# Kernel optimization log

Hardware: AMD Instinct MI355X
Metric: run time of the kernel (lower is better)

## Reference

```python
import jax, jax.numpy as jnp
import numpy as np

B, S, D, H, L, FF, V, T = 4, 160, 512, 8, 2, 2048, 50000, 256
Wd = D // H


def layer_norm(x, g, b, eps=1e-12):
    u = x.mean(-1, keepdims=True)
    s = ((x - u) ** 2).mean(-1, keepdims=True)
    return g * (x - u) / jnp.sqrt(s + eps) + b


def setup_inputs() -> dict:
    key = jax.random.key(0)
    ks = jax.random.split(key, 16)
    sc = 0.02
    inp = {
        'x': jax.random.randint(ks[0], (B, S), 0, V),
        'stamp': jax.random.randint(ks[1], (B, S - 1, 3), 0, 8),
        'mask': jnp.ones((B, S), dtype=jnp.int32),
        'time_matrix': jax.random.randint(ks[2], (B, S, S), 0, T + 1),
        'tok_emb': jax.random.normal(ks[3], (V, D)) * sc,
        'month_emb': jax.random.normal(ks[4], (13, D)) * sc,
        'day_emb': jax.random.normal(ks[5], (32, D)) * sc,
        'tiK_emb': jax.random.normal(ks[6], (T + 1, D)) * sc,
        'tiV_emb': jax.random.normal(ks[7], (T + 1, D)) * sc,
        'g0': jnp.ones((D,)), 'b0': jnp.zeros((D,)),
        'Wq': jax.random.normal(ks[8], (L, D, D)) * sc, 'bq': jnp.zeros((L, D)),
        'Wk': jax.random.normal(ks[9], (L, D, D)) * sc, 'bk': jnp.zeros((L, D)),
        'Wv': jax.random.normal(ks[10], (L, D, D)) * sc, 'bv': jnp.zeros((L, D)),
        'Wo': jax.random.normal(ks[11], (L, D, D)) * sc, 'bo': jnp.zeros((L, D)),
        'g1': jnp.ones((L, D)), 'b1': jnp.zeros((L, D)),
        'W1': jax.random.normal(ks[12], (L, D, FF)) * sc, 'c1': jnp.zeros((L, FF)),
        'W2': jax.random.normal(ks[13], (L, FF, D)) * sc, 'c2': jnp.zeros((L, D)),
        'g2': jnp.ones((L, D)), 'b2': jnp.zeros((L, D)),
    }
    return inp


def reference(x, stamp, mask, time_matrix, tok_emb, month_emb, day_emb,
              tiK_emb, tiV_emb, g0, b0, Wq, bq, Wk, bk, Wv, bv, Wo, bo,
              g1, b1, W1, c1, W2, c2, g2, b2):
    # Embeddings: month + day temporal embed, one zero timestep prepended
    t_e = month_emb[stamp[..., 0]] + day_emb[stamp[..., 1]]          # [B,S-1,D]
    t_e = jnp.concatenate([jnp.zeros((B, 1, D), t_e.dtype), t_e], axis=1)
    h = layer_norm(tok_emb[x] + t_e, g0, b0)                         # [B,S,D]
    tK = tiK_emb[time_matrix].reshape(B, S, S, H, Wd)                # [B,S,S,H,W]
    tV = tiV_emb[time_matrix].reshape(B, S, S, H, Wd)
    maskf = mask.astype(h.dtype)
    # faithful to original: +10000*(1-mask), added AFTER scaling
    bias = 10000.0 * (1.0 - maskf)[:, None, None, :]
    inv_sqrt = 1.0 / jnp.sqrt(jnp.asarray(Wd, h.dtype))
    for l in range(L):
        q = (h @ Wq[l] + bq[l]).reshape(B, S, H, Wd).transpose(0, 2, 1, 3)  # [B,H,S,W]
        k = (h @ Wk[l] + bk[l]).reshape(B, S, H, Wd).transpose(0, 2, 1, 3)
        v = (h @ Wv[l] + bv[l]).reshape(B, S, H, Wd).transpose(0, 2, 1, 3)
        scores = (jnp.einsum('bhiw,bhjw->bhij', q, k)
                  + jnp.einsum('bijhw,bhiw->bhij', tK, q)) * inv_sqrt + bias
        attn = jax.nn.softmax(scores, axis=-1)                        # [B,H,S,S]
        # standard value mix + diagonal of attn-weighted t_V (relative-time values)
        hh = (jnp.einsum('bhij,bhjw->bihw', attn, v)
              + jnp.einsum('bhik,bikhw->bihw', attn, tV)).reshape(B, S, D)
        h = layer_norm(h + hh @ Wo[l] + bo[l], g1[l], b1[l])
        ff = jax.nn.gelu(h @ W1[l] + c1[l], approximate=False) @ W2[l] + c2[l]
        h = layer_norm(h + ff, g2[l], b2[l])
    return h
```

## Files before the change

kernel.cpp:

```cpp
#include <hip/hip_runtime.h>
#include <hip/hip_bf16.h>
#include <math.h>

#define SS 160
#define DD 512
#define HH 8
#define MTOK 640
#define FFD 2048
#define NTT 257

typedef __attribute__((ext_vector_type(8))) short bfrag8;
typedef __attribute__((ext_vector_type(4))) float facc4;
typedef unsigned short u16;

#define SWZ(row, cb) ((cb) ^ (((row)&7) << 4))

__device__ __forceinline__ void gload16(const void* g, void* l) {
  __builtin_amdgcn_global_load_lds(
      (const __attribute__((address_space(1))) void*)g,
      (__attribute__((address_space(3))) void*)l, 16, 0, 0);
}

__device__ __forceinline__ u16 f2b(float f) {
  __hip_bfloat16 hb = __float2bfloat16(f);
  return *reinterpret_cast<u16*>(&hb);
}

__device__ void wconv_body(const float* __restrict__ src,
                           __hip_bfloat16* __restrict__ dst,
                           int K, int N, int dls, int rowoff,
                           int l, int bx, int by, float (*tile)[65])
{
  src += (size_t)l * K * N;
  dst += (size_t)l * dls + (size_t)rowoff * K;
  int k0 = by * 64, n0 = bx * 64;
  int t = threadIdx.x;
  int r = t >> 2, c0 = (t & 3) * 16;
  #pragma unroll
  for (int j = 0; j < 16; j += 4) {
    float4 v4 = *(const float4*)&src[(size_t)(k0 + r) * N + n0 + c0 + j];
    tile[r][c0 + j + 0] = v4.x; tile[r][c0 + j + 1] = v4.y;
    tile[r][c0 + j + 2] = v4.z; tile[r][c0 + j + 3] = v4.w;
  }
  __syncthreads();
  union { u16 u[8]; uint4 v; } pk;
  #pragma unroll
  for (int half = 0; half < 2; ++half) {
    #pragma unroll
    for (int j = 0; j < 8; ++j)
      pk.u[j] = f2b(tile[c0 + half * 8 + j][r]);
    *(uint4*)&dst[(size_t)(n0 + r) * K + k0 + c0 + half * 8] = pk.v;
  }
}

__global__ __launch_bounds__(256) void prep_all(
    const float* __restrict__ Wq, const float* __restrict__ Wk,
    const float* __restrict__ Wv, const float* __restrict__ Wo,
    const float* __restrict__ W1, const float* __restrict__ W2,
    const float* __restrict__ tiK,
    __hip_bfloat16* __restrict__ wqkv, __hip_bfloat16* __restrict__ wo_t,
    __hip_bfloat16* __restrict__ w1_t, __hip_bfloat16* __restrict__ w2_t,
    __hip_bfloat16* __restrict__ tikb,
    const int* __restrict__ x, const int* __restrict__ stamp,
    const float* __restrict__ tok, const float* __restrict__ month,
    const float* __restrict__ day, const float* __restrict__ g0,
    const float* __restrict__ b0, float* __restrict__ h,
    __hip_bfloat16* __restrict__ hb)
{
  __shared__ float tile[64][65];
  __shared__ float ssh[4], qsh[4];
  int idx = blockIdx.x;
  int tid = threadIdx.x;

  if (idx < 1536) {
    if (idx < 384) {
      int grp = idx / 128, r = idx % 128;
      int l = r / 64, t = r % 64;
      const float* src = grp == 0 ? Wq : (grp == 1 ? Wk : Wv);
      wconv_body(src, wqkv, 512, 512, 1536 * 512, 512 * grp, l, t % 8, t / 8, tile);
    } else if (idx < 512) {
      int r = idx - 384; int l = r / 64, t = r % 64;
      wconv_body(Wo, wo_t, 512, 512, 512 * 512, 0, l, t % 8, t / 8, tile);
    } else if (idx < 1024) {
      int r = idx - 512; int l = r / 256, t = r % 256;
      wconv_body(W1, w1_t, 512, 2048, 2048 * 512, 0, l, t % 32, t / 32, tile);
    } else {
      int r = idx - 1024; int l = r / 256, t = r % 256;
      wconv_body(W2, w2_t, 2048, 512, 512 * 2048, 0, l, t % 8, t / 8, tile);
    }
  } else if (idx < 1665) {
    int i = (idx - 1536) * 256 + tid;
    if (i < NTT * DD / 4) {
      float4 v = *(const float4*)(tiK + (size_t)i * 4);
      union { u16 u[4]; uint2 w; } pk;
      pk.u[0] = f2b(v.x); pk.u[1] = f2b(v.y);
      pk.u[2] = f2b(v.z); pk.u[3] = f2b(v.w);
      *(uint2*)(tikb + (size_t)i * 4) = pk.w;
    }
  } else {
    int m = idx - 1665;
    int b = m / SS, s = m % SS, t = tid;
    int tokid = x[m];
    float v0 = tok[tokid * DD + t];
    float v1 = tok[tokid * DD + t + 256];
    if (s > 0) {
      int sidx = (b * (SS - 1) + (s - 1)) * 3;
      int mo = stamp[sidx + 0], dy = stamp[sidx + 1];
      v0 += month[mo * DD + t]       + day[dy * DD + t];
      v1 += month[mo * DD + t + 256] + day[dy * DD + t + 256];
    }
    float sum = v0 + v1, sq = v0 * v0 + v1 * v1;
    #pragma unroll
    for (int off = 1; off < 64; off <<= 1) {
      sum += __shfl_xor(sum, off);
      sq  += __shfl_xor(sq , off);
    }
    if ((t & 63) == 0) { ssh[t >> 6] = sum; qsh[t >> 6] = sq; }
    __syncthreads();
    float fsum = ssh[0] + ssh[1] + ssh[2] + ssh[3];
    float fsq  = qsh[0] + qsh[1] + qsh[2] + qsh[3];
    float u = fsum * (1.0f / 512.0f);
    float var = fsq * (1.0f / 512.0f) - u * u;
    float r = rsqrtf(var + 1e-12f);
    float y0 = g0[t]       * ((v0 - u) * r) + b0[t];
    float y1 = g0[t + 256] * ((v1 - u) * r) + b0[t + 256];
    h[m * DD + t]        = y0;  h[m * DD + t + 256]  = y1;
    hb[m * DD + t]       = __float2bfloat16(y0);
    hb[m * DD + t + 256] = __float2bfloat16(y1);
  }
}

__global__ __launch_bounds__(256) void ln_kernel(
    const float* __restrict__ in, const float* __restrict__ g,
    const float* __restrict__ b, float* __restrict__ out,
    __hip_bfloat16* __restrict__ outb)
{
  int m = blockIdx.x; int t = threadIdx.x;
  float v0 = in[m*DD + t];
  float v1 = in[m*DD + t + 256];
  float sum = v0+v1, sq = v0*v0+v1*v1;
  #pragma unroll
  for (int off=1; off<64; off<<=1) {
    sum += __shfl_xor(sum, off);
    sq  += __shfl_xor(sq , off);
  }
  __shared__ float ssh[4], qsh[4];
  if ((t&63)==0) { ssh[t>>6]=sum; qsh[t>>6]=sq; }
  __syncthreads();
  float fsum = ssh[0]+ssh[1]+ssh[2]+ssh[3];
  float fsq  = qsh[0]+qsh[1]+qsh[2]+qsh[3];
  float u = fsum * (1.0f/512.0f);
  float var = fsq * (1.0f/512.0f) - u*u;
  float r = rsqrtf(var + 1e-12f);
  float y0 = g[t]    *((v0-u)*r) + b[t];
  float y1 = g[t+256]*((v1-u)*r) + b[t+256];
  out[m*DD+t]     = y0;
  out[m*DD+t+256] = y1;
  if (outb) {
    outb[m*DD+t]     = __float2bfloat16(y0);
    outb[m*DD+t+256] = __float2bfloat16(y1);
  }
}

#define EPI_RESID 1
#define EPI_GELU 2
#define EPI_QKV 3

template<int EPI, int K>
__global__ __launch_bounds__(256) void gemm_ck(
    const __hip_bfloat16* __restrict__ A,
    const __hip_bfloat16* __restrict__ Bt,
    const float* __restrict__ bias,
    const float* __restrict__ bias2,
    const float* __restrict__ bias3,
    const float* __restrict__ resid,
    float* __restrict__ Cf,
    __hip_bfloat16* __restrict__ Cb,
    int N)
{
  constexpr int KC = 128;
  constexpr int NCH = K / KC;
  __shared__ u16 As[2][64 * KC];
  __shared__ u16 Bs[2][64 * KC];
  const int tid = threadIdx.x, wv = tid >> 6, lane = tid & 63;
  const int m0 = blockIdx.y * 64, n0 = blockIdx.x * 64;
  const int wr = wv >> 1, wc = wv & 1;
  const int fr = lane & 15, fks = lane >> 4;

  const int ldsq = (wv * 4) * 1024;
  const int off0 = ldsq + lane * 16;

  #define STAGE(c, buf) do {                                                  \
    _Pragma("unroll")                                                         \
    for (int i_ = 0; i_ < 4; ++i_) {                                          \
      int ldso = ldsq + i_ * 1024;                                            \
      int off = off0 + i_ * 1024;                                             \
      int r_ = off >> 8;                                                      \
      int p_ = off & 255;                                                     \
      int ps_ = p_ ^ ((r_ & 7) << 4);                                         \
      gload16((const char*)A  + ((size_t)(m0 + r_) * K + (c) * KC) * 2 + ps_, \
              (char*)&As[buf][0] + ldso);                                     \
      gload16((const char*)Bt + ((size_t)(n0 + r_) * K + (c) * KC) * 2 + ps_, \
              (char*)&Bs[buf][0] + ldso);                                     \
    }                                                                         \
  } while (0)

  facc4 acc[2][2] = {};
  STAGE(0, 0);
  STAGE(1, 1);

  #pragma unroll
  for (int c = 0; c < NCH; ++c) {
    if (c + 1 < NCH) asm volatile("s_waitcnt vmcnt(8)\n\ts_barrier" ::: "memory");
    else             asm volatile("s_waitcnt vmcnt(0)\n\ts_barrier" ::: "memory");
    const char* ab = (const char*)&As[c & 1][0];
    const char* bb = (const char*)&Bs[c & 1][0];
    #pragma unroll
    for (int ks = 0; ks < 4; ++ks) {
      bfrag8 af[2], bfv[2];
      #pragma unroll
      for (int mf = 0; mf < 2; ++mf) {
        int rA = wr * 32 + mf * 16 + fr;
        af[mf] = *(const bfrag8*)(ab + rA * 256 + SWZ(rA, ks * 64 + fks * 16));
      }
      #pragma unroll
      for (int nf = 0; nf < 2; ++nf) {
        int rB = wc * 32 + nf * 16 + fr;
        bfv[nf] = *(const bfrag8*)(bb + rB * 256 + SWZ(rB, ks * 64 + fks * 16));
      }
      #pragma unroll
      for (int mf = 0; mf < 2; ++mf)
        #pragma unroll
        for (int nf = 0; nf < 2; ++nf)
          acc[mf][nf] = __builtin_amdgcn_mfma_f32_16x16x32_bf16(
              af[mf], bfv[nf], acc[mf][nf], 0, 0, 0);
    }
    asm volatile("s_barrier" ::: "memory");
    if (c + 2 < NCH) STAGE(c + 2, c & 1);
  }
  #undef STAGE

  #pragma unroll
  for (int mf = 0; mf < 2; ++mf) {
    #pragma unroll
    for (int nf = 0; nf < 2; ++nf) {
      int col = n0 + wc * 32 + nf * 16 + fr;
      float bb;
      if (EPI == EPI_QKV)
        bb = col < 512 ? bias[col] : (col < 1024 ? bias2[col - 512] : bias3[col - 1024]);
      else
        bb = bias[col];
      #pragma unroll
      for (int j = 0; j < 4; ++j) {
        int row = m0 + wr * 32 + mf * 16 + fks * 4 + j;
        float c = acc[mf][nf][j] + bb;
        if (EPI == EPI_RESID) {
          c += resid[(size_t)row * N + col];
          Cf[(size_t)row * N + col] = c;
        } else {
          if (EPI == EPI_GELU) c = 0.5f * c * (1.0f + erff(c * 0.70710678118654752f));
          Cb[(size_t)row * N + col] = __float2bfloat16(c);
        }
      }
    }
  }
}

__global__ __launch_bounds__(256) void attn_f(
    const __hip_bfloat16* __restrict__ qkv,
    const __hip_bfloat16* __restrict__ tikb,
    const int* __restrict__ tm, const int* __restrict__ mask,
    const float* __restrict__ tiV, __hip_bfloat16* __restrict__ hh)
{
  const int h = blockIdx.y, b = blockIdx.z;
  const int i0 = blockIdx.x * 8;
  const int tid = threadIdx.x, wv = tid >> 6, lane = tid & 63;
  const int fr = lane & 15, fks = lane >> 4;
  __shared__ float S[8][160];
  __shared__ float Gsh[8][272];
  __shared__ float P[8][176];
  __shared__ int tmsh[8][176];

  bfrag8 aq0, aq1;
  {
    const __hip_bfloat16* qrow =
        qkv + (size_t)(b * SS + i0 + (fr < 8 ? fr : 7)) * 1536 + h * 64;
    aq0 = *(const bfrag8*)(qrow + fks * 8);
    aq1 = *(const bfrag8*)(qrow + 32 + fks * 8);
  }
  for (int tt = wv; tt < 27; tt += 4) {
    facc4 acc = {};
    if (tt < 10) {
      int j = tt * 16 + fr;
      const __hip_bfloat16* krow = qkv + (size_t)(b * SS + j) * 1536 + 512 + h * 64;
      bfrag8 b0 = *(const bfrag8*)(krow + fks * 8);
      bfrag8 b1 = *(const bfrag8*)(krow + 32 + fks * 8);
      acc = __builtin_amdgcn_mfma_f32_16x16x32_bf16(aq0, b0, acc, 0, 0, 0);
      acc = __builtin_amdgcn_mfma_f32_16x16x32_bf16(aq1, b1, acc, 0, 0, 0);
      #pragma unroll
      for (int jj = 0; jj < 4; ++jj) {
        int qr = fks * 4 + jj;
        if (qr < 8) S[qr][tt * 16 + fr] = acc[jj];
      }
    } else {
      int t0 = (tt - 10) * 16;
      int t = min(t0 + fr, NTT - 1);
      const __hip_bfloat16* trow = tikb + (size_t)t * 512 + h * 64;
      bfrag8 b0 = *(const bfrag8*)(trow + fks * 8);
      bfrag8 b1 = *(const bfrag8*)(trow + 32 + fks * 8);
      acc = __builtin_amdgcn_mfma_f32_16x16x32_bf16(aq0, b0, acc, 0, 0, 0);
      acc = __builtin_amdgcn_mfma_f32_16x16x32_bf16(aq1, b1, acc, 0, 0, 0);
      #pragma unroll
      for (int jj = 0; jj < 4; ++jj) {
        int qr = fks * 4 + jj;
        if (qr < 8) Gsh[qr][t0 + fr] = acc[jj];
      }
    }
  }
  __syncthreads();

  float rinvs[2];
  #pragma unroll
  for (int rr = 0; rr < 2; ++rr) {
    const int r = wv * 2 + rr, i = i0 + r, m = b * SS + i;
    const int* tmrow = tm + (size_t)m * SS;
    float sv[3];
    float mx = -1e30f;
    #pragma unroll
    for (int g = 0; g < 3; ++g) {
      int j = lane + g * 64;
      if (j < SS) {
        int t = tmrow[j];
        tmsh[r][j] = t;
        float s = (S[r][j] + Gsh[r][t]) * 0.125f
                + 10000.0f * (1.0f - (float)mask[b * SS + j]);
        sv[g] = s; mx = fmaxf(mx, s);
      } else sv[g] = -1e30f;
    }
    #pragma unroll
    for (int off = 1; off < 64; off <<= 1) mx = fmaxf(mx, __shfl_xor(mx, off));
    float sum = 0.f;
    #pragma unroll
    for (int g = 0; g < 3; ++g) {
      int j = lane + g * 64;
      if (j < SS) { float p = expf(sv[g] - mx); P[r][j] = p; sum += p; }
    }
    #pragma unroll
    for (int off = 1; off < 64; off <<= 1) sum += __shfl_xor(sum, off);
    rinvs[rr] = 1.0f / sum;
  }

  const int r0 = wv * 2, r1 = r0 + 1;
  const int ii0 = i0 + r0, ii1 = i0 + r1;
  const __hip_bfloat16* vbase = qkv + (size_t)b * SS * 1536 + 1024 + h * 64 + lane;
  const float* tvbase = tiV + h * 64 + lane;
  float acc0 = 0.f, acc1 = 0.f;
  #pragma unroll 4
  for (int j = 0; j < SS; ++j) {
    float vv = __bfloat162float(vbase[(size_t)j * 1536]);
    float a0 = P[r0][j], a1 = P[r1][j];
    int t0 = tmsh[r0][j], t1 = tmsh[r1][j];
    acc0 += a0 * (vv + tvbase[(size_t)t0 * 512]);
    acc1 += a1 * (vv + tvbase[(size_t)t1 * 512]);
  }
  hh[((size_t)(b * SS) + ii0) * DD + h * 64 + lane] = __float2bfloat16(acc0 * rinvs[0]);
  hh[((size_t)(b * SS) + ii1) * DD + h * 64 + lane] = __float2bfloat16(acc1 * rinvs[1]);
}

extern "C" void kernel_launch(void* const* d_in, const int* in_sizes, int n_in,
                              void* d_out, int out_size, void* d_ws, size_t ws_size,
                              hipStream_t stream) {
  const int*   x     = (const int*)d_in[0];
  const int*   stamp = (const int*)d_in[1];
  const int*   mask  = (const int*)d_in[2];
  const int*   tm    = (const int*)d_in[3];
  const float* tok   = (const float*)d_in[4];
  const float* month = (const float*)d_in[5];
  const float* day   = (const float*)d_in[6];
  const float* tiK   = (const float*)d_in[7];
  const float* tiV   = (const float*)d_in[8];
  const float* g0    = (const float*)d_in[9];
  const float* b0    = (const float*)d_in[10];
  const float* Wq    = (const float*)d_in[11];
  const float* bq    = (const float*)d_in[12];
  const float* Wk    = (const float*)d_in[13];
  const float* bk    = (const float*)d_in[14];
  const float* Wv    = (const float*)d_in[15];
  const float* bv    = (const float*)d_in[16];
  const float* Wo    = (const float*)d_in[17];
  const float* bo    = (const float*)d_in[18];
  const float* g1    = (const float*)d_in[19];
  const float* b1    = (const float*)d_in[20];
  const float* W1    = (const float*)d_in[21];
  const float* c1    = (const float*)d_in[22];
  const float* W2    = (const float*)d_in[23];
  const float* c2    = (const float*)d_in[24];
  const float* g2    = (const float*)d_in[25];
  const float* b2    = (const float*)d_in[26];

  float* out = (float*)d_out;
  const size_t NT = (size_t)MTOK * DD;

  char* p = (char*)d_ws;
  float* h    = (float*)p;  p += NT * 4;
  float* tb   = (float*)p;  p += NT * 4;
  __hip_bfloat16* h_bf   = (__hip_bfloat16*)p;  p += NT * 2;
  __hip_bfloat16* hh_bf  = (__hip_bfloat16*)p;  p += NT * 2;
  __hip_bfloat16* fb_bf  = (__hip_bfloat16*)p;  p += (size_t)MTOK * FFD * 2;
  __hip_bfloat16* qkv_bf = (__hip_bfloat16*)p;  p += (size_t)MTOK * 1536 * 2;
  __hip_bfloat16* tikb   = (__hip_bfloat16*)p;  p += (size_t)NTT * DD * 2;
  __hip_bfloat16* wqkv   = (__hip_bfloat16*)p;  p += (size_t)2 * 1536 * 512 * 2;
  __hip_bfloat16* wo_t   = (__hip_bfloat16*)p;  p += (size_t)2 * 512 * 512 * 2;
  __hip_bfloat16* w1_t   = (__hip_bfloat16*)p;  p += (size_t)2 * 2048 * 512 * 2;
  __hip_bfloat16* w2_t   = (__hip_bfloat16*)p;  p += (size_t)2 * 512 * 2048 * 2;

  prep_all<<<2305, 256, 0, stream>>>(Wq, Wk, Wv, Wo, W1, W2, tiK,
                                     wqkv, wo_t, w1_t, w2_t, tikb,
                                     x, stamp, tok, month, day, g0, b0, h, h_bf);

  for (int l = 0; l < 2; ++l) {
    gemm_ck<EPI_QKV, 512><<<dim3(24, 10), 256, 0, stream>>>(
        h_bf, wqkv + (size_t)l * 1536 * 512, bq + l*DD, bk + l*DD, bv + l*DD,
        nullptr, nullptr, qkv_bf, 1536);

    attn_f<<<dim3(20, 8, 4), 256, 0, stream>>>(qkv_bf, tikb, tm, mask, tiV, hh_bf);

    gemm_ck<EPI_RESID, 512><<<dim3(8, 10), 256, 0, stream>>>(
        hh_bf, wo_t + (size_t)l * 512 * 512, bo + l*DD, nullptr, nullptr,
        h, tb, nullptr, 512);
    ln_kernel<<<MTOK, 256, 0, stream>>>(tb, g1 + l*DD, b1 + l*DD, h, h_bf);

    gemm_ck<EPI_GELU, 512><<<dim3(32, 10), 256, 0, stream>>>(
        h_bf, w1_t + (size_t)l * 2048 * 512, c1 + l*FFD, nullptr, nullptr,
        nullptr, nullptr, fb_bf, 2048);

    gemm_ck<EPI_RESID, 2048><<<dim3(8, 10), 256, 0, stream>>>(
        fb_bf, w2_t + (size_t)l * 512 * 2048, c2 + l*DD, nullptr, nullptr,
        h, tb, nullptr, 512);
    ln_kernel<<<MTOK, 256, 0, stream>>>(tb, g2 + l*DD, b2 + l*DD,
                                        (l == 1) ? out : h,
                                        (l == 1) ? nullptr : h_bf);
  }
}
```

Measured before the change: 146.3 us.

## Split-K the N=512 GEMMs and fold partial reduction into layernorm

The Wo and W2 projections (N=512) launched only 80 blocks, which underfills the GPU. They now run as split-K over 4 K-slices with 320 blocks, each writing fp32 partials. A new layernorm kernel sums the four partials plus bias and residual before normalizing. This trades extra partial-buffer traffic (4x fp32 writes and reads) for more parallelism in these GEMMs.

```diff
diff --git a/kernel.cpp b/kernel.cpp
--- a/kernel.cpp
+++ b/kernel.cpp
@@ -8,6 +8,7 @@
 #define MTOK 640
 #define FFD 2048
 #define NTT 257
+#define NTE (MTOK * DD)
 
 typedef __attribute__((ext_vector_type(8))) short bfrag8;
 typedef __attribute__((ext_vector_type(4))) float facc4;
@@ -130,43 +131,51 @@
   }
 }
 
-__global__ __launch_bounds__(256) void ln_kernel(
-    const float* __restrict__ in, const float* __restrict__ g,
-    const float* __restrict__ b, float* __restrict__ out,
-    __hip_bfloat16* __restrict__ outb)
+__global__ __launch_bounds__(256) void ln_red(
+    const float* __restrict__ parts,
+    const float* __restrict__ resid,
+    const float* __restrict__ bias,
+    const float* __restrict__ g, const float* __restrict__ b,
+    float* __restrict__ out, __hip_bfloat16* __restrict__ outb)
 {
   int m = blockIdx.x; int t = threadIdx.x;
-  float v0 = in[m*DD + t];
-  float v1 = in[m*DD + t + 256];
-  float sum = v0+v1, sq = v0*v0+v1*v1;
-  #pragma unroll
-  for (int off=1; off<64; off<<=1) {
+  float v0 = bias[t]       + resid[(size_t)m * DD + t];
+  float v1 = bias[t + 256] + resid[(size_t)m * DD + t + 256];
+  #pragma unroll
+  for (int s = 0; s < 4; ++s) {
+    v0 += parts[(size_t)s * NTE + (size_t)m * DD + t];
+    v1 += parts[(size_t)s * NTE + (size_t)m * DD + t + 256];
+  }
+  float sum = v0 + v1, sq = v0 * v0 + v1 * v1;
+  #pragma unroll
+  for (int off = 1; off < 64; off <<= 1) {
     sum += __shfl_xor(sum, off);
     sq  += __shfl_xor(sq , off);
   }
   __shared__ float ssh[4], qsh[4];
-  if ((t&63)==0) { ssh[t>>6]=sum; qsh[t>>6]=sq; }
+  if ((t & 63) == 0) { ssh[t >> 6] = sum; qsh[t >> 6] = sq; }
   __syncthreads();
-  float fsum = ssh[0]+ssh[1]+ssh[2]+ssh[3];
-  float fsq  = qsh[0]+qsh[1]+qsh[2]+qsh[3];
-  float u = fsum * (1.0f/512.0f);
-  float var = fsq * (1.0f/512.0f) - u*u;
+  float fsum = ssh[0] + ssh[1] + ssh[2] + ssh[3];
+  float fsq  = qsh[0] + qsh[1] + qsh[2] + qsh[3];
+  float u = fsum * (1.0f / 512.0f);
+  float var = fsq * (1.0f / 512.0f) - u * u;
   float r = rsqrtf(var + 1e-12f);
-  float y0 = g[t]    *((v0-u)*r) + b[t];
-  float y1 = g[t+256]*((v1-u)*r) + b[t+256];
-  out[m*DD+t]     = y0;
-  out[m*DD+t+256] = y1;
+  float y0 = g[t]       * ((v0 - u) * r) + b[t];
+  float y1 = g[t + 256] * ((v1 - u) * r) + b[t + 256];
+  out[(size_t)m * DD + t]       = y0;
+  out[(size_t)m * DD + t + 256] = y1;
   if (outb) {
-    outb[m*DD+t]     = __float2bfloat16(y0);
-    outb[m*DD+t+256] = __float2bfloat16(y1);
+    outb[(size_t)m * DD + t]       = __float2bfloat16(y0);
+    outb[(size_t)m * DD + t + 256] = __float2bfloat16(y1);
   }
 }
 
 #define EPI_RESID 1
 #define EPI_GELU 2
 #define EPI_QKV 3
-
-template<int EPI, int K>
+#define EPI_PART 4
+
+template<int EPI, int KEXT, int KSTRIDE>
 __global__ __launch_bounds__(256) void gemm_ck(
     const __hip_bfloat16* __restrict__ A,
     const __hip_bfloat16* __restrict__ Bt,
@@ -176,16 +185,20 @@
     const float* __restrict__ resid,
     float* __restrict__ Cf,
     __hip_bfloat16* __restrict__ Cb,
-    int N)
+    int N, int pstride)
 {
   constexpr int KC = 128;
-  constexpr int NCH = K / KC;
+  constexpr int NCH = KEXT / KC;
   __shared__ u16 As[2][64 * KC];
   __shared__ u16 Bs[2][64 * KC];
   const int tid = threadIdx.x, wv = tid >> 6, lane = tid & 63;
   const int m0 = blockIdx.y * 64, n0 = blockIdx.x * 64;
+  const int kz = blockIdx.z;
   const int wr = wv >> 1, wc = wv & 1;
   const int fr = lane & 15, fks = lane >> 4;
+
+  A  += (size_t)kz * KEXT;
+  Bt += (size_t)kz * KEXT;
 
   const int ldsq = (wv * 4) * 1024;
   const int off0 = ldsq + lane * 16;
@@ -198,16 +211,16 @@
       int r_ = off >> 8;                                                      \
       int p_ = off & 255;                                                     \
       int ps_ = p_ ^ ((r_ & 7) << 4);                                         \
-      gload16((const char*)A  + ((size_t)(m0 + r_) * K + (c) * KC) * 2 + ps_, \
+      gload16((const char*)A  + ((size_t)(m0 + r_) * KSTRIDE + (c) * KC) * 2 + ps_, \
               (char*)&As[buf][0] + ldso);                                     \
-      gload16((const char*)Bt + ((size_t)(n0 + r_) * K + (c) * KC) * 2 + ps_, \
+      gload16((const char*)Bt + ((size_t)(n0 + r_) * KSTRIDE + (c) * KC) * 2 + ps_, \
               (char*)&Bs[buf][0] + ldso);                                     \
     }                                                                         \
   } while (0)
 
   facc4 acc[2][2] = {};
   STAGE(0, 0);
-  STAGE(1, 1);
+  if (NCH > 1) STAGE(1, 1);
 
   #pragma unroll
   for (int c = 0; c < NCH; ++c) {
@@ -245,16 +258,18 @@
     #pragma unroll
     for (int nf = 0; nf < 2; ++nf) {
       int col = n0 + wc * 32 + nf * 16 + fr;
-      float bb;
+      float bb2 = 0.f;
       if (EPI == EPI_QKV)
-        bb = col < 512 ? bias[col] : (col < 1024 ? bias2[col - 512] : bias3[col - 1024]);
-      else
-        bb = bias[col];
+        bb2 = col < 512 ? bias[col] : (col < 1024 ? bias2[col - 512] : bias3[col - 1024]);
+      else if (EPI != EPI_PART)
+        bb2 = bias[col];
       #pragma unroll
       for (int j = 0; j < 4; ++j) {
         int row = m0 + wr * 32 + mf * 16 + fks * 4 + j;
-        float c = acc[mf][nf][j] + bb;
-        if (EPI == EPI_RESID) {
+        float c = acc[mf][nf][j] + bb2;
+        if (EPI == EPI_PART) {
+          Cf[(size_t)kz * pstride + (size_t)row * N + col] = c;
+        } else if (EPI == EPI_RESID) {
           c += resid[(size_t)row * N + col];
           Cf[(size_t)row * N + col] = c;
         } else {
@@ -403,7 +418,7 @@
 
   char* p = (char*)d_ws;
   float* h    = (float*)p;  p += NT * 4;
-  float* tb   = (float*)p;  p += NT * 4;
+  float* tbp  = (float*)p;  p += (size_t)4 * NT * 4;
   __hip_bfloat16* h_bf   = (__hip_bfloat16*)p;  p += NT * 2;
   __hip_bfloat16* hh_bf  = (__hip_bfloat16*)p;  p += NT * 2;
   __hip_bfloat16* fb_bf  = (__hip_bfloat16*)p;  p += (size_t)MTOK * FFD * 2;
@@ -419,26 +434,28 @@
                                      x, stamp, tok, month, day, g0, b0, h, h_bf);
 
   for (int l = 0; l < 2; ++l) {
-    gemm_ck<EPI_QKV, 512><<<dim3(24, 10), 256, 0, stream>>>(
+    gemm_ck<EPI_QKV, 512, 512><<<dim3(24, 10), 256, 0, stream>>>(
         h_bf, wqkv + (size_t)l * 1536 * 512, bq + l*DD, bk + l*DD, bv + l*DD,
-        nullptr, nullptr, qkv_bf, 1536);
+        nullptr, nullptr, qkv_bf, 1536, 0);
 
     attn_f<<<dim3(20, 8, 4), 256, 0, stream>>>(qkv_bf, tikb, tm, mask, tiV, hh_bf);
 
-    gemm_ck<EPI_RESID, 512><<<dim3(8, 10), 256, 0, stream>>>(
-        hh_bf, wo_t + (size_t)l * 512 * 512, bo + l*DD, nullptr, nullptr,
-        h, tb, nullptr, 512);
-    ln_kernel<<<MTOK, 256, 0, stream>>>(tb, g1 + l*DD, b1 + l*DD, h, h_bf);
-
-    gemm_ck<EPI_GELU, 512><<<dim3(32, 10), 256, 0, stream>>>(
+    gemm_ck<EPI_PART, 128, 512><<<dim3(8, 10, 4), 256, 0, stream>>>(
+        hh_bf, wo_t + (size_t)l * 512 * 512, nullptr, nullptr, nullptr,
+        nullptr, tbp, nullptr, 512, (int)NT);
+    ln_red<<<MTOK, 256, 0, stream>>>(tbp, h, bo + l*DD,
+                                     g1 + l*DD, b1 + l*DD, h, h_bf);
+
+    gemm_ck<EPI_GELU, 512, 512><<<dim3(32, 10), 256, 0, stream>>>(
         h_bf, w1_t + (size_t)l * 2048 * 512, c1 + l*FFD, nullptr, nullptr,
-        nullptr, nullptr, fb_bf, 2048);
-
-    gemm_ck<EPI_RESID, 2048><<<dim3(8, 10), 256, 0, stream>>>(
-        fb_bf, w2_t + (size_t)l * 512 * 2048, c2 + l*DD, nullptr, nullptr,
-        h, tb, nullptr, 512);
-    ln_kernel<<<MTOK, 256, 0, stream>>>(tb, g2 + l*DD, b2 + l*DD,
-                                        (l == 1) ? out : h,
-                                        (l == 1) ? nullptr : h_bf);
-  }
-}
+        nullptr, nullptr, fb_bf, 2048, 0);
+
+    gemm_ck<EPI_PART, 512, 2048><<<dim3(8, 10, 4), 256, 0, stream>>>(
+        fb_bf, w2_t + (size_t)l * 512 * 2048, nullptr, nullptr, nullptr,
+        nullptr, tbp, nullptr, 512, (int)NT);
+    ln_red<<<MTOK, 256, 0, stream>>>(tbp, h, c2 + l*DD,
+                                     g2 + l*DD, b2 + l*DD,
+                                     (l == 1) ? out : h,
+                                     (l == 1) ? nullptr : h_bf);
+  }
+}
```

After: 128.7 us. 12.0% less time.
